# Optimization experiments

Hardware: AMD Instinct MI355X
Metric: run time of the kernel (lower is better)

## Reference

```python
import jax, jax.numpy as jnp
from jax import lax
import numpy as np

ALPHA = 0.5
MAX_ITERS = 40
TOL = 1e-6
BITS = 8


def fake_quant_sym(w, bits=BITS):
    # symmetric per-tensor fake quantisation
    qmax = float(2 ** (bits - 1) - 1)
    scale = jnp.max(jnp.abs(w)) / qmax
    return jnp.round(w / scale) * scale


def fb_solve(Wq, Uq, bq, x, alpha=ALPHA, max_iters=MAX_ITERS, tol=TOL):
    # forward-backward splitting fixed-point solve: z = relu((1-a)z + a(Wz + Ux^T + b))
    n = Wq.shape[0]
    B = x.shape[0]
    Ux = Uq @ x.T + bq[:, None]  # (n, B), constant across iterations

    def cond(carry):
        z, res, it = carry
        return jnp.logical_and(it < max_iters, res >= tol)

    def body(carry):
        z, _, it = carry
        u = (1.0 - alpha) * z + alpha * (Wq @ z + Ux)
        z_next = jax.nn.relu(u)  # relu_prox
        res = jnp.linalg.norm(z_next - z) / (jnp.linalg.norm(z) + 1e-12)
        return z_next, res, it + 1

    z0 = jnp.zeros((n, B), dtype=x.dtype)
    z, _, _ = lax.while_loop(cond, body, (z0, jnp.array(jnp.inf, dtype=x.dtype), 0))
    u_star = (1.0 - alpha) * z + alpha * (Wq @ z + Ux)
    mask = (u_star > 0).astype(x.dtype)  # relu Jacobian mask D*
    return z, mask


def setup_inputs() -> dict:
    key = jax.random.key(0)
    k0, k1, k2, k3, k4 = jax.random.split(key, 5)
    n, d, B, C = 512, 784, 128, 10
    # scale W so ||W||_2 < 1 (monotone operator condition m > 0)
    W = 0.3 * jax.random.normal(k0, (n, n), dtype=jnp.float32) / jnp.sqrt(n)
    U = jax.random.normal(k1, (n, d), dtype=jnp.float32) / jnp.sqrt(d)
    b = 0.01 * jax.random.normal(k2, (n,), dtype=jnp.float32)
    x = jax.random.normal(k3, (B, d), dtype=jnp.float32)
    Wc = jax.random.normal(k4, (C, n), dtype=jnp.float32) / jnp.sqrt(n)
    bc = jnp.zeros((C,), dtype=jnp.float32)
    return {"W": W, "U": U, "b": b, "x": x, "Wc": Wc, "bc": bc}


def reference(W, U, b, x, Wc, bc):
    # post-training fake quantisation of W, U, b (done once at init in torch)
    Wq = fake_quant_sym(W)
    Uq = fake_quant_sym(U)
    bq = fake_quant_sym(b)
    z_star, _ = fb_solve(Wq, Uq, bq, x)  # (n, B)
    logits = z_star.T @ Wc.T + bc  # classifier on z*^T
    return logits
```

## Files before the change

kernel.cpp:

```cpp
#include <hip/hip_runtime.h>
#include <hip/hip_bf16.h>


#define N_DIM 512
#define D_DIM 784
#define B_DIM 128
#define C_DIM 10
#define QMAX 127.0f
#define N_ITERS 40
#define HILO_START 28
#define ZPITCH 528
#define MT 4
#define UPITCH 808

typedef int    i32x4  __attribute__((ext_vector_type(4)));
typedef float  f32x4  __attribute__((ext_vector_type(4)));
typedef __bf16 bf16x8 __attribute__((ext_vector_type(8)));

__device__ __forceinline__ float pscale64(const float* __restrict__ p) {
    float m = 0.0f;
#pragma unroll 16
    for (int i = 0; i < 64; ++i) m = fmaxf(m, p[i]);
    return m * (1.0f / QMAX);
}

__global__ void maxabs_kernel(const float* __restrict__ W,
                              const float* __restrict__ U,
                              const float* __restrict__ b,
                              float* __restrict__ partials) {
    const float4* src;
    int n4;
    if (blockIdx.y == 0)      { src = (const float4*)W; n4 = N_DIM * N_DIM / 4; }
    else if (blockIdx.y == 1) { src = (const float4*)U; n4 = N_DIM * D_DIM / 4; }
    else                      { src = (const float4*)b; n4 = N_DIM / 4; }
    float m = 0.0f;
    for (int i = blockIdx.x * blockDim.x + threadIdx.x; i < n4; i += gridDim.x * blockDim.x) {
        float4 v = src[i];
        m = fmaxf(m, fmaxf(fmaxf(fabsf(v.x), fabsf(v.y)), fmaxf(fabsf(v.z), fabsf(v.w))));
    }
    __shared__ float red[256];
    red[threadIdx.x] = m;
    __syncthreads();
    for (int s = 128; s > 0; s >>= 1) {
        if (threadIdx.x < s) red[threadIdx.x] = fmaxf(red[threadIdx.x], red[threadIdx.x + s]);
        __syncthreads();
    }
    if (threadIdx.x == 0) partials[blockIdx.y * 64 + blockIdx.x] = red[0];
}

__global__ __launch_bounds__(256) void prep_kernel(const float* __restrict__ W,
                                                   const float* __restrict__ U,
                                                   const float* __restrict__ b,
                                                   const float* __restrict__ x,
                                                   const float* __restrict__ partials,
                                                   int* __restrict__ rowsum,
                                                   signed char* __restrict__ Qp8,
                                                   float* __restrict__ UxT) {
    __shared__ __bf16 uS[16][UPITCH];
    __shared__ __bf16 xhS[16][UPITCH];
    __shared__ __bf16 xlS[16][UPITCH];
    __shared__ f32x4  sacc[4][64];
    __shared__ int ls[4];
    const int t = threadIdx.x;
    if (blockIdx.x < 256) {
        const float s = pscale64(partials);
        const float inv = 1.0f / s;
        int idx = blockIdx.x * 256 + t;
        float4 w = ((const float4*)W)[idx];
        int k = (idx << 2) & (N_DIM - 1);
        int r = (idx << 2) >> 9;
        int q0 = (int)rintf(w.x * inv);
        int q1 = (int)rintf(w.y * inv);
        int q2 = (int)rintf(w.z * inv);
        int q3 = (int)rintf(w.w * inv);
        char4 c;
        c.x = (signed char)q0; c.y = (signed char)q1;
        c.z = (signed char)q2; c.w = (signed char)q3;
        int kc = k >> 6, q = (k >> 4) & 3, jj = k & 15;
        *(char4*)&Qp8[((kc << 9) + r) * 64 + q * 16 + jj] = c;
        int psum = q0 + q1 + q2 + q3;
#pragma unroll
        for (int s2 = 1; s2 < 64; s2 <<= 1) psum += __shfl_xor(psum, s2);
        if ((t & 63) == 0) ls[t >> 6] = psum;
        __syncthreads();
        if (t == 0) {
            rowsum[2 * blockIdx.x]     = ls[0] + ls[1];
            rowsum[2 * blockIdx.x + 1] = ls[2] + ls[3];
        }
    } else {
        const float sU = pscale64(partials + 64);
        const float invU = 1.0f / sU;
        const float sb = pscale64(partials + 128);
        const int bx = blockIdx.x - 256;
        const int i0 = (bx >> 3) * 16;
        const int c0 = (bx & 7) * 16;
        for (int r = 0; r < 16; ++r) {
            for (int k = t; k < D_DIM; k += 256) {
                float uv = U[(i0 + r) * D_DIM + k];
                uS[r][k] = (__bf16)rintf(uv * invU);
                float xv = x[(c0 + r) * D_DIM + k];
                __bf16 h = (__bf16)xv;
                xhS[r][k] = h;
                xlS[r][k] = (__bf16)(xv - (float)h);
            }
        }
        for (int i = t; i < 16 * 16; i += 256) {
            int r = i >> 4, k = D_DIM + (i & 15);
            uS[r][k] = (__bf16)0.0f; xhS[r][k] = (__bf16)0.0f; xlS[r][k] = (__bf16)0.0f;
        }
        __syncthreads();
        const int wave = t >> 6, lane = t & 63;
        const int m = lane & 15, quad = lane >> 4;
        f32x4 acc = {};
        for (int kc = wave; kc < 25; kc += 4) {
            bf16x8 a  = *(const bf16x8*)&uS[m][kc * 32 + (quad << 3)];
            bf16x8 bh = *(const bf16x8*)&xhS[m][kc * 32 + (quad << 3)];
            bf16x8 bl = *(const bf16x8*)&xlS[m][kc * 32 + (quad << 3)];
            acc = __builtin_amdgcn_mfma_f32_16x16x32_bf16(a, bh, acc, 0, 0, 0);
            acc = __builtin_amdgcn_mfma_f32_16x16x32_bf16(a, bl, acc, 0, 0, 0);
        }
        sacc[wave][lane] = acc;
        __syncthreads();
        if (wave == 0) {
            f32x4 s0 = sacc[0][lane], s1 = sacc[1][lane];
            f32x4 s2 = sacc[2][lane], s3 = sacc[3][lane];
            const int row0 = i0 + (quad << 2);
            f32x4 o;
#pragma unroll
            for (int r = 0; r < 4; ++r)
                o[r] = sU * (s0[r] + s1[r] + s2[r] + s3[r])
                     + rintf(b[row0 + r] / sb) * sb;
            *(f32x4*)&UxT[(c0 + m) * N_DIM + row0] = o;
        }
    }
}

__global__ __launch_bounds__(512, 2) void solve_kernel(const signed char* __restrict__ Qp8,
                                                       const float* __restrict__ UxT,
                                                       const float* __restrict__ partials,
                                                       const int* __restrict__ rowsum,
                                                       const float* __restrict__ Wc,
                                                       const float* __restrict__ bc,
                                                       float* __restrict__ out) {
    __shared__ signed char zh[2][16][ZPITCH];
    __shared__ signed char zl[2][16][ZPITCH];
    __shared__ float red[32][16][C_DIM];
    const int t = threadIdx.x;
    const int wave = t >> 6;
    const int lane = t & 63;
    const int m = lane & 15;
    const int quad = lane >> 4;
    const int c0 = blockIdx.x * 16;
    const float sW = pscale64(partials);
    const float c1 = sW * (1.0f / 2048.0f);
    const float hc_hi = c1 * 128.0f;
    const float hc_lo = c1 * 0.5f;

    const int rowbase = wave * 64;
    float zreg[MT][4];
    float uxh[MT][4];
#pragma unroll
    for (int ti = 0; ti < MT; ++ti) {
        const int row0 = rowbase + ti * 16 + (quad << 2);
        int vq[4];
#pragma unroll
        for (int r = 0; r < 4; ++r) {
            float v = UxT[(c0 + m) * N_DIM + row0 + r];
            uxh[ti][r] = 0.5f * (v + c1 * 128.0f * (float)rowsum[row0 + r]);
            float z1 = fmaxf(0.5f * v, 0.0f);
            zreg[ti][r] = z1;
            vq[r] = min((int)rintf(z1 * 2048.0f), 32767);
        }
        unsigned int h = (unsigned int)(vq[0] >> 8) | ((unsigned int)(vq[1] >> 8) << 8)
                       | ((unsigned int)(vq[2] >> 8) << 16) | ((unsigned int)(vq[3] >> 8) << 24);
        unsigned int l = (unsigned int)(vq[0] & 255) | ((unsigned int)(vq[1] & 255) << 8)
                       | ((unsigned int)(vq[2] & 255) << 16) | ((unsigned int)(vq[3] & 255) << 24);
        *(unsigned int*)&zh[0][m][row0] = h;
        *(unsigned int*)&zl[0][m][row0] = l ^ 0x80808080u;
    }

    i32x4 A[MT][8];
#pragma unroll
    for (int ti = 0; ti < MT; ++ti)
#pragma unroll
        for (int kc = 0; kc < 8; ++kc)
            A[ti][kc] = *(const i32x4*)&Qp8[((kc << 9) + rowbase + ti * 16 + m) * 64 + (quad << 4)];
#pragma unroll
    for (int ti = 0; ti < MT; ++ti)
#pragma unroll
        for (int kc = 0; kc < 8; ++kc)
            asm volatile("" : "+v"(A[ti][kc]));
    __syncthreads();

    int cur = 0;
    for (int it = 1; it < N_ITERS; ++it) {
        const bool lo = (it >= HILO_START);
        const bool wlo = (it >= HILO_START - 1);
        i32x4 acch[MT] = {};
        i32x4 accl[MT] = {};
        if (lo) {
#pragma unroll
            for (int kc = 0; kc < 8; ++kc) {
                i32x4 bh = *(const i32x4*)&zh[cur][m][(kc << 6) + (quad << 4)];
                i32x4 bl = *(const i32x4*)&zl[cur][m][(kc << 6) + (quad << 4)];
#pragma unroll
                for (int ti = 0; ti < MT; ++ti) {
                    acch[ti] = __builtin_amdgcn_mfma_i32_16x16x64_i8(A[ti][kc], bh, acch[ti], 0, 0, 0);
                    accl[ti] = __builtin_amdgcn_mfma_i32_16x16x64_i8(A[ti][kc], bl, accl[ti], 0, 0, 0);
                }
            }
        } else {
#pragma unroll
            for (int kc = 0; kc < 8; ++kc) {
                i32x4 bh = *(const i32x4*)&zh[cur][m][(kc << 6) + (quad << 4)];
#pragma unroll
                for (int ti = 0; ti < MT; ++ti)
                    acch[ti] = __builtin_amdgcn_mfma_i32_16x16x64_i8(A[ti][kc], bh, acch[ti], 0, 0, 0);
            }
        }
        const int nxt = cur ^ 1;
#pragma unroll
        for (int ti = 0; ti < MT; ++ti) {
            const int row0 = rowbase + ti * 16 + (quad << 2);
            int vq[4];
#pragma unroll
            for (int r = 0; r < 4; ++r) {
                float base = fmaf(0.5f, zreg[ti][r], uxh[ti][r]);
                float u = lo ? fmaf(hc_hi, (float)acch[ti][r], fmaf(hc_lo, (float)accl[ti][r], base))
                             : fmaf(hc_hi, (float)acch[ti][r], base);
                float zn = fmaxf(u, 0.0f);
                zreg[ti][r] = zn;
                vq[r] = min((int)rintf(zn * 2048.0f), 32767);
            }
            unsigned int h = (unsigned int)(vq[0] >> 8) | ((unsigned int)(vq[1] >> 8) << 8)
                           | ((unsigned int)(vq[2] >> 8) << 16) | ((unsigned int)(vq[3] >> 8) << 24);
            *(unsigned int*)&zh[nxt][m][row0] = h;
            if (wlo) {
                unsigned int l = (unsigned int)(vq[0] & 255) | ((unsigned int)(vq[1] & 255) << 8)
                               | ((unsigned int)(vq[2] & 255) << 16) | ((unsigned int)(vq[3] & 255) << 24);
                *(unsigned int*)&zl[nxt][m][row0] = l ^ 0x80808080u;
            }
        }
        __syncthreads();
        cur = nxt;
    }

    {
        const int grp = wave * 4 + quad;
        float p[C_DIM];
#pragma unroll
        for (int cl = 0; cl < C_DIM; ++cl) p[cl] = 0.0f;
#pragma unroll
        for (int ti = 0; ti < MT; ++ti) {
            const int row0 = rowbase + ti * 16 + (quad << 2);
#pragma unroll
            for (int r = 0; r < 4; ++r) {
                float zv = zreg[ti][r];
#pragma unroll
                for (int cl = 0; cl < C_DIM; ++cl)
                    p[cl] += zv * Wc[cl * N_DIM + row0 + r];
            }
        }
#pragma unroll
        for (int cl = 0; cl < C_DIM; ++cl) red[grp][m][cl] = p[cl];
        __syncthreads();
        for (int s = 16; s > 0; s >>= 1) {
            if (grp < s) {
#pragma unroll
                for (int cl = 0; cl < C_DIM; ++cl)
                    red[grp][m][cl] += red[grp + s][m][cl];
            }
            __syncthreads();
        }
        if (t < 16 * C_DIM) {
            int col = t & 15;
            int cl  = t >> 4;
            out[(c0 + col) * C_DIM + cl] = red[0][col][cl] + bc[cl];
        }
    }
}

extern "C" void kernel_launch(void* const* d_in, const int* in_sizes, int n_in,
                              void* d_out, int out_size, void* d_ws, size_t ws_size,
                              hipStream_t stream) {
    const float* W  = (const float*)d_in[0];
    const float* U  = (const float*)d_in[1];
    const float* b  = (const float*)d_in[2];
    const float* x  = (const float*)d_in[3];
    const float* Wc = (const float*)d_in[4];
    const float* bc = (const float*)d_in[5];
    float* out = (float*)d_out;

    float* ws = (float*)d_ws;
    float* partials = ws;
    int* rowsum = (int*)(ws + 256);
    signed char* Qp8 = (signed char*)(ws + 256 + 512);
    float* UxT = ws + 256 + 512 + (N_DIM * N_DIM / 4);

    maxabs_kernel<<<dim3(64, 3), 256, 0, stream>>>(W, U, b, partials);
    prep_kernel<<<512, 256, 0, stream>>>(W, U, b, x, partials, rowsum, Qp8, UxT);
    solve_kernel<<<8, 512, 0, stream>>>(Qp8, UxT, partials, rowsum, Wc, bc, out);
}
```

Measured before the change: 158.7 us.

## Compute W row sums via MFMA in solver and streamline prep packing

Removes the rowsum reduction and its workspace from the prep kernel. The solver now computes the row sums itself with int8 MFMAs against a ones vector, reusing the quantised W fragments it already loads. The prep kernel quantises U directly from global memory into MFMA operands instead of staging it in shared memory, and converts x with vectorised float4 loads. The z hi/lo byte packing now uses cvt_pk_i16 plus perm instead of shift/mask chains, and the 32767 clamp is dropped, which relies on z values staying within range.

```diff
diff --git a/kernel.cpp b/kernel.cpp
--- a/kernel.cpp
+++ b/kernel.cpp
@@ -16,12 +16,28 @@
 typedef int    i32x4  __attribute__((ext_vector_type(4)));
 typedef float  f32x4  __attribute__((ext_vector_type(4)));
 typedef __bf16 bf16x8 __attribute__((ext_vector_type(8)));
+typedef short  s16x2  __attribute__((ext_vector_type(2)));
 
 __device__ __forceinline__ float pscale64(const float* __restrict__ p) {
     float m = 0.0f;
 #pragma unroll 16
     for (int i = 0; i < 64; ++i) m = fmaxf(m, p[i]);
     return m * (1.0f / QMAX);
+}
+
+__device__ __forceinline__ void pack_hl(const int vq[4], unsigned int& h, unsigned int& l) {
+    int pk01, pk23;
+#if __has_builtin(__builtin_amdgcn_cvt_pk_i16)
+    union { s16x2 v; int i; } u0, u1;
+    u0.v = __builtin_amdgcn_cvt_pk_i16(vq[0], vq[1]);
+    u1.v = __builtin_amdgcn_cvt_pk_i16(vq[2], vq[3]);
+    pk01 = u0.i; pk23 = u1.i;
+#else
+    asm("v_cvt_pk_i16_i32 %0, %1, %2" : "=v"(pk01) : "v"(vq[0]), "v"(vq[1]));
+    asm("v_cvt_pk_i16_i32 %0, %1, %2" : "=v"(pk23) : "v"(vq[2]), "v"(vq[3]));
+#endif
+    h = __builtin_amdgcn_perm((unsigned int)pk23, (unsigned int)pk01, 0x07050301u);
+    l = __builtin_amdgcn_perm((unsigned int)pk23, (unsigned int)pk01, 0x06040200u) ^ 0x80808080u;
 }
 
 __global__ void maxabs_kernel(const float* __restrict__ W,
@@ -53,14 +69,11 @@
                                                    const float* __restrict__ b,
                                                    const float* __restrict__ x,
                                                    const float* __restrict__ partials,
-                                                   int* __restrict__ rowsum,
                                                    signed char* __restrict__ Qp8,
                                                    float* __restrict__ UxT) {
-    __shared__ __bf16 uS[16][UPITCH];
     __shared__ __bf16 xhS[16][UPITCH];
     __shared__ __bf16 xlS[16][UPITCH];
     __shared__ f32x4  sacc[4][64];
-    __shared__ int ls[4];
     const int t = threadIdx.x;
     if (blockIdx.x < 256) {
         const float s = pscale64(partials);
@@ -69,24 +82,13 @@
         float4 w = ((const float4*)W)[idx];
         int k = (idx << 2) & (N_DIM - 1);
         int r = (idx << 2) >> 9;
-        int q0 = (int)rintf(w.x * inv);
-        int q1 = (int)rintf(w.y * inv);
-        int q2 = (int)rintf(w.z * inv);
-        int q3 = (int)rintf(w.w * inv);
         char4 c;
-        c.x = (signed char)q0; c.y = (signed char)q1;
-        c.z = (signed char)q2; c.w = (signed char)q3;
+        c.x = (signed char)(int)rintf(w.x * inv);
+        c.y = (signed char)(int)rintf(w.y * inv);
+        c.z = (signed char)(int)rintf(w.z * inv);
+        c.w = (signed char)(int)rintf(w.w * inv);
         int kc = k >> 6, q = (k >> 4) & 3, jj = k & 15;
         *(char4*)&Qp8[((kc << 9) + r) * 64 + q * 16 + jj] = c;
-        int psum = q0 + q1 + q2 + q3;
-#pragma unroll
-        for (int s2 = 1; s2 < 64; s2 <<= 1) psum += __shfl_xor(psum, s2);
-        if ((t & 63) == 0) ls[t >> 6] = psum;
-        __syncthreads();
-        if (t == 0) {
-            rowsum[2 * blockIdx.x]     = ls[0] + ls[1];
-            rowsum[2 * blockIdx.x + 1] = ls[2] + ls[3];
-        }
     } else {
         const float sU = pscale64(partials + 64);
         const float invU = 1.0f / sU;
@@ -94,30 +96,43 @@
         const int bx = blockIdx.x - 256;
         const int i0 = (bx >> 3) * 16;
         const int c0 = (bx & 7) * 16;
-        for (int r = 0; r < 16; ++r) {
-            for (int k = t; k < D_DIM; k += 256) {
-                float uv = U[(i0 + r) * D_DIM + k];
-                uS[r][k] = (__bf16)rintf(uv * invU);
-                float xv = x[(c0 + r) * D_DIM + k];
-                __bf16 h = (__bf16)xv;
-                xhS[r][k] = h;
-                xlS[r][k] = (__bf16)(xv - (float)h);
-            }
-        }
-        for (int i = t; i < 16 * 16; i += 256) {
-            int r = i >> 4, k = D_DIM + (i & 15);
-            uS[r][k] = (__bf16)0.0f; xhS[r][k] = (__bf16)0.0f; xlS[r][k] = (__bf16)0.0f;
+        for (int i = t; i < 16 * 196; i += 256) {
+            int r = i / 196, kf = i - r * 196;
+            float4 v = *(const float4*)&x[(c0 + r) * D_DIM + (kf << 2)];
+            union { __bf16 e[4]; ushort4 u; } hh, ll;
+            float f0 = v.x, f1 = v.y, f2 = v.z, f3 = v.w;
+            __bf16 h0 = (__bf16)f0, h1 = (__bf16)f1, h2 = (__bf16)f2, h3 = (__bf16)f3;
+            hh.e[0] = h0; hh.e[1] = h1; hh.e[2] = h2; hh.e[3] = h3;
+            ll.e[0] = (__bf16)(f0 - (float)h0);
+            ll.e[1] = (__bf16)(f1 - (float)h1);
+            ll.e[2] = (__bf16)(f2 - (float)h2);
+            ll.e[3] = (__bf16)(f3 - (float)h3);
+            *(ushort4*)&xhS[r][kf << 2] = hh.u;
+            *(ushort4*)&xlS[r][kf << 2] = ll.u;
+        }
+        {
+            int r = t >> 4, k = D_DIM + (t & 15);
+            xhS[r][k] = (__bf16)0.0f; xlS[r][k] = (__bf16)0.0f;
         }
         __syncthreads();
         const int wave = t >> 6, lane = t & 63;
         const int m = lane & 15, quad = lane >> 4;
         f32x4 acc = {};
         for (int kc = wave; kc < 25; kc += 4) {
-            bf16x8 a  = *(const bf16x8*)&uS[m][kc * 32 + (quad << 3)];
-            bf16x8 bh = *(const bf16x8*)&xhS[m][kc * 32 + (quad << 3)];
-            bf16x8 bl = *(const bf16x8*)&xlS[m][kc * 32 + (quad << 3)];
-            acc = __builtin_amdgcn_mfma_f32_16x16x32_bf16(a, bh, acc, 0, 0, 0);
-            acc = __builtin_amdgcn_mfma_f32_16x16x32_bf16(a, bl, acc, 0, 0, 0);
+            const int k0 = (kc << 5) + (quad << 3);
+            bf16x8 au = {};
+            if (k0 < D_DIM) {
+                const float4 u0 = *(const float4*)&U[(i0 + m) * D_DIM + k0];
+                const float4 u1 = *(const float4*)&U[(i0 + m) * D_DIM + k0 + 4];
+                au[0] = (__bf16)rintf(u0.x * invU); au[1] = (__bf16)rintf(u0.y * invU);
+                au[2] = (__bf16)rintf(u0.z * invU); au[3] = (__bf16)rintf(u0.w * invU);
+                au[4] = (__bf16)rintf(u1.x * invU); au[5] = (__bf16)rintf(u1.y * invU);
+                au[6] = (__bf16)rintf(u1.z * invU); au[7] = (__bf16)rintf(u1.w * invU);
+            }
+            bf16x8 bh = *(const bf16x8*)&xhS[m][k0];
+            bf16x8 bl = *(const bf16x8*)&xlS[m][k0];
+            acc = __builtin_amdgcn_mfma_f32_16x16x32_bf16(au, bh, acc, 0, 0, 0);
+            acc = __builtin_amdgcn_mfma_f32_16x16x32_bf16(au, bl, acc, 0, 0, 0);
         }
         sacc[wave][lane] = acc;
         __syncthreads();
@@ -138,7 +153,6 @@
 __global__ __launch_bounds__(512, 2) void solve_kernel(const signed char* __restrict__ Qp8,
                                                        const float* __restrict__ UxT,
                                                        const float* __restrict__ partials,
-                                                       const int* __restrict__ rowsum,
                                                        const float* __restrict__ Wc,
                                                        const float* __restrict__ bc,
                                                        float* __restrict__ out) {
@@ -155,36 +169,47 @@
     const float c1 = sW * (1.0f / 2048.0f);
     const float hc_hi = c1 * 128.0f;
     const float hc_lo = c1 * 0.5f;
-
     const int rowbase = wave * 64;
+
+    i32x4 A[MT][8];
+#pragma unroll
+    for (int ti = 0; ti < MT; ++ti)
+#pragma unroll
+        for (int kc = 0; kc < 8; ++kc)
+            A[ti][kc] = *(const i32x4*)&Qp8[((kc << 9) + rowbase + ti * 16 + m) * 64 + (quad << 4)];
+
+    const i32x4 onesb = {0x01010101, 0x01010101, 0x01010101, 0x01010101};
+    i32x4 rs[MT];
+#pragma unroll
+    for (int ti = 0; ti < MT; ++ti) {
+        i32x4 a = {};
+#pragma unroll
+        for (int kc = 0; kc < 8; ++kc)
+            a = __builtin_amdgcn_mfma_i32_16x16x64_i8(A[ti][kc], onesb, a, 0, 0, 0);
+        rs[ti] = a;
+    }
+
     float zreg[MT][4];
     float uxh[MT][4];
 #pragma unroll
     for (int ti = 0; ti < MT; ++ti) {
         const int row0 = rowbase + ti * 16 + (quad << 2);
+        const f32x4 v4 = *(const f32x4*)&UxT[(c0 + m) * N_DIM + row0];
         int vq[4];
 #pragma unroll
         for (int r = 0; r < 4; ++r) {
-            float v = UxT[(c0 + m) * N_DIM + row0 + r];
-            uxh[ti][r] = 0.5f * (v + c1 * 128.0f * (float)rowsum[row0 + r]);
-            float z1 = fmaxf(0.5f * v, 0.0f);
+            const float v = v4[r];
+            uxh[ti][r] = 0.5f * (v + hc_hi * (float)rs[ti][r]);
+            const float z1 = fmaxf(0.5f * v, 0.0f);
             zreg[ti][r] = z1;
-            vq[r] = min((int)rintf(z1 * 2048.0f), 32767);
-        }
-        unsigned int h = (unsigned int)(vq[0] >> 8) | ((unsigned int)(vq[1] >> 8) << 8)
-                       | ((unsigned int)(vq[2] >> 8) << 16) | ((unsigned int)(vq[3] >> 8) << 24);
-        unsigned int l = (unsigned int)(vq[0] & 255) | ((unsigned int)(vq[1] & 255) << 8)
-                       | ((unsigned int)(vq[2] & 255) << 16) | ((unsigned int)(vq[3] & 255) << 24);
+            vq[r] = (int)rintf(z1 * 2048.0f);
+        }
+        unsigned int h, l;
+        pack_hl(vq, h, l);
         *(unsigned int*)&zh[0][m][row0] = h;
-        *(unsigned int*)&zl[0][m][row0] = l ^ 0x80808080u;
-    }
-
-    i32x4 A[MT][8];
-#pragma unroll
-    for (int ti = 0; ti < MT; ++ti)
-#pragma unroll
-        for (int kc = 0; kc < 8; ++kc)
-            A[ti][kc] = *(const i32x4*)&Qp8[((kc << 9) + rowbase + ti * 16 + m) * 64 + (quad << 4)];
+        *(unsigned int*)&zl[0][m][row0] = l;
+    }
+
 #pragma unroll
     for (int ti = 0; ti < MT; ++ti)
 #pragma unroll
@@ -230,16 +255,12 @@
                              : fmaf(hc_hi, (float)acch[ti][r], base);
                 float zn = fmaxf(u, 0.0f);
                 zreg[ti][r] = zn;
-                vq[r] = min((int)rintf(zn * 2048.0f), 32767);
-            }
-            unsigned int h = (unsigned int)(vq[0] >> 8) | ((unsigned int)(vq[1] >> 8) << 8)
-                           | ((unsigned int)(vq[2] >> 8) << 16) | ((unsigned int)(vq[3] >> 8) << 24);
+                vq[r] = (int)rintf(zn * 2048.0f);
+            }
+            unsigned int h, l;
+            pack_hl(vq, h, l);
             *(unsigned int*)&zh[nxt][m][row0] = h;
-            if (wlo) {
-                unsigned int l = (unsigned int)(vq[0] & 255) | ((unsigned int)(vq[1] & 255) << 8)
-                               | ((unsigned int)(vq[2] & 255) << 16) | ((unsigned int)(vq[3] & 255) << 24);
-                *(unsigned int*)&zl[nxt][m][row0] = l ^ 0x80808080u;
-            }
+            if (wlo) *(unsigned int*)&zl[nxt][m][row0] = l;
         }
         __syncthreads();
         cur = nxt;
@@ -293,11 +314,10 @@
 
     float* ws = (float*)d_ws;
     float* partials = ws;
-    int* rowsum = (int*)(ws + 256);
-    signed char* Qp8 = (signed char*)(ws + 256 + 512);
-    float* UxT = ws + 256 + 512 + (N_DIM * N_DIM / 4);
+    signed char* Qp8 = (signed char*)(ws + 256);
+    float* UxT = ws + 256 + (N_DIM * N_DIM / 4);
 
     maxabs_kernel<<<dim3(64, 3), 256, 0, stream>>>(W, U, b, partials);
-    prep_kernel<<<512, 256, 0, stream>>>(W, U, b, x, partials, rowsum, Qp8, UxT);
-    solve_kernel<<<8, 512, 0, stream>>>(Qp8, UxT, partials, rowsum, Wc, bc, out);
-}
+    prep_kernel<<<512, 256, 0, stream>>>(W, U, b, x, partials, Qp8, UxT);
+    solve_kernel<<<8, 512, 0, stream>>>(Qp8, UxT, partials, Wc, bc, out);
+}
```

New measurement: 142.3 us. -10.3%, faster.
